# Kernel optimization log

Hardware: AMD Instinct MI355X
Metric: run time of the kernel (lower is better)

## Reference

```python
import jax, jax.numpy as jnp
import numpy as np

NUM_QUBITS = 10
NUM_LAYERS = 5
OBS = 10          # observation_size == num_qubits (required by input_scaling indexing)
NUM_OUTPUTS = 4   # num_actions, discretize=False
BATCH = 4096


def _bcast(theta, n):
    # theta: scalar or (B,) -> broadcastable against (B, 2, 2, ..., 2)
    return jnp.reshape(jnp.asarray(theta), (-1,) + (1,) * n)


def _ry(st, theta, q, n):
    # st: (B,) + (2,)*n complex64; per-sample RY(theta) on qubit q
    t = _bcast(theta, n) * 0.5
    c, s = jnp.cos(t), jnp.sin(t)
    s0 = jax.lax.index_in_dim(st, 0, axis=q + 1, keepdims=True)
    s1 = jax.lax.index_in_dim(st, 1, axis=q + 1, keepdims=True)
    return jnp.concatenate([c * s0 - s * s1, s * s0 + c * s1], axis=q + 1)


def _rz(st, theta, q, n):
    t = _bcast(theta, n) * 0.5
    s0 = jax.lax.index_in_dim(st, 0, axis=q + 1, keepdims=True)
    s1 = jax.lax.index_in_dim(st, 1, axis=q + 1, keepdims=True)
    return jnp.concatenate([jnp.exp(-1j * t) * s0, jnp.exp(1j * t) * s1], axis=q + 1)


def _cnot(st, c, t):
    # flip target axis on the control=1 slab; pure index ops (no residuals in bwd)
    s0 = jax.lax.index_in_dim(st, 0, axis=c + 1, keepdims=True)
    s1 = jax.lax.index_in_dim(st, 1, axis=c + 1, keepdims=True)
    s1 = jnp.flip(s1, axis=t + 1)
    return jnp.concatenate([s0, s1], axis=c + 1)


def _layer(st, x, isc, w, n, obs):
    # isc: (2n,) input_scaling row, w: (2n,) weights row
    for i in range(obs):
        st = _ry(st, isc[i] * x[:, i], i, n)
        st = _rz(st, isc[i + obs] * x[:, i], i, n)
    for i in range(n):
        st = _rz(st, w[i], i, n)
    for i in range(n):
        st = _ry(st, w[i + n], i, n)
    if n == 2:
        st = _cnot(st, 0, 1)
    else:
        for i in range(n):
            st = _cnot(st, i, (i + 1) % n)
    return st


_layer_ckpt = jax.checkpoint(_layer, static_argnums=(4, 5))


def _circuit(x, input_scaling, weights, n, num_layers, obs, num_outputs):
    B = x.shape[0]
    st = jnp.zeros((B,) + (2,) * n, dtype=jnp.complex64)
    st = st.at[(slice(None),) + (0,) * n].set(1.0)  # |0...0>
    for layer in range(num_layers):
        st = _layer_ckpt(st, x, input_scaling[layer], weights[layer], n, obs)
    probs = jnp.real(st * jnp.conj(st))
    outs = []
    for i in range(num_outputs):
        axes = tuple(a for a in range(1, n + 1) if a != i + 1)
        pi = jnp.sum(probs, axis=axes)  # (B, 2)
        outs.append(pi[:, 0] - pi[:, 1])  # <Z_i>
    return jnp.stack(outs, axis=1)


def setup_inputs() -> dict:
    key = jax.random.key(0)
    k1, k2 = jax.random.split(key)
    x = jax.random.normal(k1, (BATCH, OBS), dtype=jnp.float32)
    input_scaling = jnp.ones((NUM_LAYERS, 2 * NUM_QUBITS), dtype=jnp.float32)
    weights = jax.random.uniform(k2, (NUM_LAYERS, 2 * NUM_QUBITS), minval=-np.pi, maxval=np.pi, dtype=jnp.float32)
    output_scaling = jnp.ones((NUM_OUTPUTS,), dtype=jnp.float32)
    return {"x": x, "input_scaling": input_scaling, "weights": weights, "output_scaling": output_scaling}


def reference(x, input_scaling, weights, output_scaling):
    z = _circuit(x, input_scaling, weights, NUM_QUBITS, NUM_LAYERS, OBS, NUM_OUTPUTS)
    return z * output_scaling  # (B, num_actions); discretize=False -> actions = scaled expvals
```

## Files before the change

kernel.cpp:

```cpp
#include <hip/hip_runtime.h>


constexpr int NQ  = 10;
constexpr int NL  = 5;
constexpr int OBS = 10;

typedef float f2 __attribute__((ext_vector_type(2)));

__device__ __forceinline__ float readlane_f(float v, int l) {
    return __int_as_float(__builtin_amdgcn_readlane(__float_as_int(v), l));
}
__device__ __forceinline__ float bperm_f(int byte_addr, float v) {
    return __int_as_float(__builtin_amdgcn_ds_bpermute(byte_addr, __float_as_int(v)));
}
template <int CTRL>
__device__ __forceinline__ float dpp_f(float v) {
    return __int_as_float(__builtin_amdgcn_update_dpp(
        0, __float_as_int(v), CTRL, 0xF, 0xF, true));
}
__device__ __forceinline__ float xor_lane(float v, int M,
                                          int a4, int a16, int a32) {
    switch (M) {
    case 1:  return dpp_f<0xB1>(v);
    case 2:  return dpp_f<0x4E>(v);
    case 8:  return dpp_f<0x128>(v);
    case 4:  return bperm_f(a4,  v);
    case 16: return bperm_f(a16, v);
    default: return bperm_f(a32, v);
    }
}

__global__ __launch_bounds__(256, 4) void qsim_kernel(
    const float* __restrict__ x,
    const float* __restrict__ isc,
    const float* __restrict__ w,
    const float* __restrict__ oscale,
    float* __restrict__ out,
    int B)
{
    const int lane = threadIdx.x & 63;
    const int wid  = (blockIdx.x * blockDim.x + threadIdx.x) >> 6;
    if (wid >= B) return;

    float cUR, cUI, cVR, cVI;
    {
        const int g   = (lane < 50) ? lane : 49;
        const int q   = g % 10;
        const int lyr = g / 10;
        const float xq    = x[wid * OBS + q];
        const float alpha = isc[lyr * 2 * NQ + q]      * xq;
        const float beta  = isc[lyr * 2 * NQ + NQ + q] * xq;
        const float gamma = w[lyr * 2 * NQ + q];
        const float delta = w[lyr * 2 * NQ + NQ + q];
        float sa, ca, sp, cp, sd, cd;
        __sincosf(0.5f * alpha,          &sa, &ca);
        __sincosf(0.5f * (beta + gamma), &sp, &cp);
        __sincosf(0.5f * delta,          &sd, &cd);
        const float A = cd * ca, Bt = sd * sa;
        const float C = cd * sa, D  = sd * ca;
        cUR = (A - Bt) * cp;
        cUI = -(A + Bt) * sp;
        cVR = (C + D) * cp;
        cVI = (C - D) * sp;
    }

    const int a4  = (lane ^ 4)  * 4;
    const int a16 = (lane ^ 16) * 4;
    const int a32 = (lane ^ 32) * 4;
    const int cnot_src  = (lane ^ (lane >> 1));
    const int addr_even = cnot_src * 4;
    const int addr_odd  = (cnot_src ^ 32) * 4;

    f2 c[16];
#pragma unroll
    for (int r = 0; r < 16; ++r) c[r] = (f2){0.f, 0.f};
    c[0].x = (lane == 0) ? 1.f : 0.f;

#define SWAPR(i, j) { f2 _t = c[i]; c[i] = c[j]; c[j] = _t; }

    for (int layer = 0; layer < NL; ++layer) {
        const int base = layer * NQ;

#pragma unroll
        for (int q = 0; q < NQ; ++q) {
            const float ur = readlane_f(cUR, base + q);
            const float ui = readlane_f(cUI, base + q);
            const float vr = readlane_f(cVR, base + q);
            const float vi = readlane_f(cVI, base + q);

            if (q < 4) {
                const f2 kUU  = {ur, ur};
                const f2 kUIm = {-ui, ui};
                const f2 kVVn = {-vr, -vr};
                const f2 kVV  = {vr, vr};
                const f2 kVIm = {-vi, vi};
                const f2 kUIp = {ui, -ui};
                const int m = 1 << (3 - q);
#pragma unroll
                for (int r0 = 0; r0 < 16; ++r0) {
                    if (r0 & m) continue;
                    const int r1 = r0 | m;
                    const f2 c0 = c[r0], c1 = c[r1];
                    const f2 c0s = c0.yx, c1s = c1.yx;
                    c[r0] = kUU*c0 + kUIm*c0s + kVVn*c1 + kVIm*c1s;
                    c[r1] = kVV*c0 + kVIm*c0s + kUU*c1  + kUIp*c1s;
                }
            } else {
                const int  M   = 1 << (9 - q);
                const bool bit = (lane & M) != 0;
                const float Pi = bit ? -ui : ui;
                const float Qr = bit ?  vr : -vr;
                const f2 kUU = {ur, ur};
                const f2 kPI = {-Pi, Pi};
                const f2 kQR = {Qr, Qr};
                const f2 kVI = {-vi, vi};
#pragma unroll
                for (int r = 0; r < 16; ++r) {
                    const f2 mv = c[r];
                    f2 pv;
                    pv.x = xor_lane(mv.x, M, a4, a16, a32);
                    pv.y = xor_lane(mv.y, M, a4, a16, a32);
                    c[r] = kUU*mv + kPI*mv.yx + kQR*pv + kVI*pv.yx;
                }
            }
        }

        SWAPR(8, 12) SWAPR(9, 13) SWAPR(10, 14) SWAPR(11, 15)
        SWAPR(4, 6)  SWAPR(5, 7)  SWAPR(12, 14) SWAPR(13, 15)
        SWAPR(2, 3)  SWAPR(6, 7)  SWAPR(10, 11) SWAPR(14, 15)
#pragma unroll
        for (int r = 0; r < 16; ++r) {
            const int addr = (r & 1) ? addr_odd : addr_even;
            c[r].x = bperm_f(addr, c[r].x);
            c[r].y = bperm_f(addr, c[r].y);
        }
        {
            const bool ctl = (lane & 1) != 0;
#pragma unroll
            for (int r = 0; r < 8; ++r) {
                const f2 t0 = c[r], t1 = c[r + 8];
                c[r]     = ctl ? t1 : t0;
                c[r + 8] = ctl ? t0 : t1;
            }
        }
    }

    float z0 = 0.f, z1 = 0.f, z2 = 0.f, z3 = 0.f;
#pragma unroll
    for (int r = 0; r < 16; ++r) {
        const float pv = c[r].x * c[r].x + c[r].y * c[r].y;
        z0 += (r & 8) ? -pv : pv;
        z1 += (r & 4) ? -pv : pv;
        z2 += (r & 2) ? -pv : pv;
        z3 += (r & 1) ? -pv : pv;
    }
#pragma unroll
    for (int m = 1; m < 64; m <<= 1) {
        z0 += xor_lane(z0, m, a4, a16, a32);
        z1 += xor_lane(z1, m, a4, a16, a32);
        z2 += xor_lane(z2, m, a4, a16, a32);
        z3 += xor_lane(z3, m, a4, a16, a32);
    }
    if (lane == 0) {
        out[wid * 4 + 0] = z0 * oscale[0];
        out[wid * 4 + 1] = z1 * oscale[1];
        out[wid * 4 + 2] = z2 * oscale[2];
        out[wid * 4 + 3] = z3 * oscale[3];
    }
#undef SWAPR
}

extern "C" void kernel_launch(void* const* d_in, const int* in_sizes, int n_in,
                              void* d_out, int out_size, void* d_ws, size_t ws_size,
                              hipStream_t stream) {
    const float* x      = (const float*)d_in[0];
    const float* isc    = (const float*)d_in[1];
    const float* w      = (const float*)d_in[2];
    const float* oscale = (const float*)d_in[3];
    float* out = (float*)d_out;

    const int B = in_sizes[0] / OBS;
    const int threads = 256;
    const int blocks = (B * 64 + threads - 1) / threads;
    qsim_kernel<<<blocks, threads, 0, stream>>>(x, isc, w, oscale, out, B);
}
```

Baseline: 97.32 us.

## Split each sample's state vector across two wavefronts with LDS exchange

Each sample is now handled by a 128-thread block of two wavefronts. Each wavefront holds half the amplitudes (8 registers instead of 16), and the top qubit's gate is applied through a shared-memory exchange between the two halves. The CNOT control swap on qubit 0 is folded into that exchange, and the final expectation values are combined through shared memory. This halves register pressure and doubles the thread count per sample to raise occupancy and parallelism, at the cost of __syncthreads barriers, LDS traffic and some redundant coefficient computation.

```diff
diff --git a/kernel.cpp b/kernel.cpp
--- a/kernel.cpp
+++ b/kernel.cpp
@@ -30,17 +30,19 @@
     }
 }
 
-__global__ __launch_bounds__(256, 4) void qsim_kernel(
+__global__ __launch_bounds__(128, 8) void qsim_kernel(
     const float* __restrict__ x,
     const float* __restrict__ isc,
     const float* __restrict__ w,
     const float* __restrict__ oscale,
-    float* __restrict__ out,
-    int B)
+    float* __restrict__ out)
 {
+    __shared__ f2    sh[1024];
+    __shared__ float red[8];
+
     const int lane = threadIdx.x & 63;
-    const int wid  = (blockIdx.x * blockDim.x + threadIdx.x) >> 6;
-    if (wid >= B) return;
+    const int h    = threadIdx.x >> 6;
+    const int wid  = blockIdx.x;
 
     float cUR, cUI, cVR, cVI;
     {
@@ -71,33 +73,73 @@
     const int addr_even = cnot_src * 4;
     const int addr_odd  = (cnot_src ^ 32) * 4;
 
-    f2 c[16];
-#pragma unroll
-    for (int r = 0; r < 16; ++r) c[r] = (f2){0.f, 0.f};
-    c[0].x = (lane == 0) ? 1.f : 0.f;
+    f2 c[8];
+#pragma unroll
+    for (int r = 0; r < 8; ++r) c[r] = (f2){0.f, 0.f};
+    if (h == 0) c[0].x = (lane == 0) ? 1.f : 0.f;
 
 #define SWAPR(i, j) { f2 _t = c[i]; c[i] = c[j]; c[j] = _t; }
 
     for (int layer = 0; layer < NL; ++layer) {
         const int base = layer * NQ;
 
-#pragma unroll
-        for (int q = 0; q < NQ; ++q) {
+        {
+            const float ur = readlane_f(cUR, base + 0);
+            const float ui = readlane_f(cUI, base + 0);
+            const float vr = readlane_f(cVR, base + 0);
+            const float vi = readlane_f(cVI, base + 0);
+            const f2 kUU  = {ur, ur};
+            const f2 kUIm = {-ui, ui};
+            const f2 kVVn = {-vr, -vr};
+            const f2 kVV  = {vr, vr};
+            const f2 kVIm = {-vi, vi};
+            const f2 kUIp = {ui, -ui};
+
+#pragma unroll
+            for (int r = 0; r < 8; ++r) sh[h * 512 + r * 64 + lane] = c[r];
+            __syncthreads();
+            f2 p[8];
+#pragma unroll
+            for (int r = 0; r < 8; ++r) p[r] = sh[(1 - h) * 512 + r * 64 + lane];
+            __syncthreads();
+
+            const bool swp = (layer != 0) && ((lane & 1) != 0);
+            if (h == 0) {
+#pragma unroll
+                for (int r = 0; r < 8; ++r) {
+                    const f2 a = c[r], b = p[r];
+                    const f2 X0 = swp ? b : a;
+                    const f2 X1 = swp ? a : b;
+                    c[r] = kUU*X0 + kUIm*X0.yx + kVVn*X1 + kVIm*X1.yx;
+                }
+            } else {
+#pragma unroll
+                for (int r = 0; r < 8; ++r) {
+                    const f2 a = c[r], b = p[r];
+                    const f2 X0 = swp ? a : b;
+                    const f2 X1 = swp ? b : a;
+                    c[r] = kVV*X0 + kVIm*X0.yx + kUU*X1 + kUIp*X1.yx;
+                }
+            }
+        }
+
+#pragma unroll
+        for (int q = 1; q < NQ; ++q) {
             const float ur = readlane_f(cUR, base + q);
             const float ui = readlane_f(cUI, base + q);
             const float vr = readlane_f(cVR, base + q);
             const float vi = readlane_f(cVI, base + q);
+            const f2 kUU  = {ur, ur};
+            const f2 kUIm = {-ui, ui};
+            const f2 kVVn = {-vr, -vr};
+            const f2 kVV  = {vr, vr};
+            const f2 kVIm = {-vi, vi};
+            const f2 kUIp = {ui, -ui};
 
             if (q < 4) {
-                const f2 kUU  = {ur, ur};
-                const f2 kUIm = {-ui, ui};
-                const f2 kVVn = {-vr, -vr};
-                const f2 kVV  = {vr, vr};
-                const f2 kVIm = {-vi, vi};
-                const f2 kUIp = {ui, -ui};
                 const int m = 1 << (3 - q);
 #pragma unroll
-                for (int r0 = 0; r0 < 16; ++r0) {
+                for (int r0 = 0; r0 < 8; ++r0) {
                     if (r0 & m) continue;
                     const int r1 = r0 | m;
                     const f2 c0 = c[r0], c1 = c[r1];
@@ -110,46 +152,38 @@
                 const bool bit = (lane & M) != 0;
                 const float Pi = bit ? -ui : ui;
                 const float Qr = bit ?  vr : -vr;
-                const f2 kUU = {ur, ur};
-                const f2 kPI = {-Pi, Pi};
-                const f2 kQR = {Qr, Qr};
-                const f2 kVI = {-vi, vi};
-#pragma unroll
-                for (int r = 0; r < 16; ++r) {
+                const f2 kUUb = {ur, ur};
+                const f2 kPI  = {-Pi, Pi};
+                const f2 kQR  = {Qr, Qr};
+                const f2 kVIb = {-vi, vi};
+#pragma unroll
+                for (int r = 0; r < 8; ++r) {
                     const f2 mv = c[r];
                     f2 pv;
                     pv.x = xor_lane(mv.x, M, a4, a16, a32);
                     pv.y = xor_lane(mv.y, M, a4, a16, a32);
-                    c[r] = kUU*mv + kPI*mv.yx + kQR*pv + kVI*pv.yx;
+                    c[r] = kUUb*mv + kPI*mv.yx + kQR*pv + kVIb*pv.yx;
                 }
             }
         }
 
-        SWAPR(8, 12) SWAPR(9, 13) SWAPR(10, 14) SWAPR(11, 15)
-        SWAPR(4, 6)  SWAPR(5, 7)  SWAPR(12, 14) SWAPR(13, 15)
-        SWAPR(2, 3)  SWAPR(6, 7)  SWAPR(10, 11) SWAPR(14, 15)
-#pragma unroll
-        for (int r = 0; r < 16; ++r) {
+        if (h) { SWAPR(0, 4) SWAPR(1, 5) SWAPR(2, 6) SWAPR(3, 7) }
+        SWAPR(4, 6) SWAPR(5, 7)
+        SWAPR(2, 3) SWAPR(6, 7)
+#pragma unroll
+        for (int r = 0; r < 8; ++r) {
             const int addr = (r & 1) ? addr_odd : addr_even;
             c[r].x = bperm_f(addr, c[r].x);
             c[r].y = bperm_f(addr, c[r].y);
         }
-        {
-            const bool ctl = (lane & 1) != 0;
-#pragma unroll
-            for (int r = 0; r < 8; ++r) {
-                const f2 t0 = c[r], t1 = c[r + 8];
-                c[r]     = ctl ? t1 : t0;
-                c[r + 8] = ctl ? t0 : t1;
-            }
-        }
-    }
-
+    }
+
+    const float s0 = ((h ^ (lane & 1)) ? -1.f : 1.f);
     float z0 = 0.f, z1 = 0.f, z2 = 0.f, z3 = 0.f;
 #pragma unroll
-    for (int r = 0; r < 16; ++r) {
+    for (int r = 0; r < 8; ++r) {
         const float pv = c[r].x * c[r].x + c[r].y * c[r].y;
-        z0 += (r & 8) ? -pv : pv;
+        z0 += s0 * pv;
         z1 += (r & 4) ? -pv : pv;
         z2 += (r & 2) ? -pv : pv;
         z3 += (r & 1) ? -pv : pv;
@@ -162,10 +196,17 @@
         z3 += xor_lane(z3, m, a4, a16, a32);
     }
     if (lane == 0) {
-        out[wid * 4 + 0] = z0 * oscale[0];
-        out[wid * 4 + 1] = z1 * oscale[1];
-        out[wid * 4 + 2] = z2 * oscale[2];
-        out[wid * 4 + 3] = z3 * oscale[3];
+        red[h * 4 + 0] = z0;
+        red[h * 4 + 1] = z1;
+        red[h * 4 + 2] = z2;
+        red[h * 4 + 3] = z3;
+    }
+    __syncthreads();
+    if (h == 0 && lane == 0) {
+        out[wid * 4 + 0] = (red[0] + red[4]) * oscale[0];
+        out[wid * 4 + 1] = (red[1] + red[5]) * oscale[1];
+        out[wid * 4 + 2] = (red[2] + red[6]) * oscale[2];
+        out[wid * 4 + 3] = (red[3] + red[7]) * oscale[3];
     }
 #undef SWAPR
 }
@@ -180,7 +221,5 @@
     float* out = (float*)d_out;
 
     const int B = in_sizes[0] / OBS;
-    const int threads = 256;
-    const int blocks = (B * 64 + threads - 1) / threads;
-    qsim_kernel<<<blocks, threads, 0, stream>>>(x, isc, w, oscale, out, B);
-}
+    qsim_kernel<<<B, 128, 0, stream>>>(x, isc, w, oscale, out);
+}
```

Result: no change. 99.02 us (+1.7%).

## Build first layer as product state and fold final CNOT ring into readout parities

Applied to the files above, without the earlier changes.

The first layer's single-qubit rotations act on |0…0>, so the state is built directly as a tensor product: each lane computes its phase from qubits 4-9, then qubits 0-3 expand across registers. This removes the butterfly and cross-lane shuffles of layer 0. The last layer's CNOT ring is dropped, and its effect on the Z expectations is absorbed by computing parity-based signs over register and lane bits. In exchange, the readout sign logic becomes more intricate and correctness depends on the parity mapping being exact.

```diff
diff --git a/kernel.cpp b/kernel.cpp
--- a/kernel.cpp
+++ b/kernel.cpp
@@ -72,69 +72,99 @@
     const int addr_odd  = (cnot_src ^ 32) * 4;
 
     f2 c[16];
-#pragma unroll
-    for (int r = 0; r < 16; ++r) c[r] = (f2){0.f, 0.f};
-    c[0].x = (lane == 0) ? 1.f : 0.f;
+
+    {
+        float Lr = 1.f, Li = 0.f;
+#pragma unroll
+        for (int q = 4; q < 10; ++q) {
+            const float ur = readlane_f(cUR, q), ui = readlane_f(cUI, q);
+            const float vr = readlane_f(cVR, q), vi = readlane_f(cVI, q);
+            const int M = 1 << (9 - q);
+            const float fr = (lane & M) ? vr : ur;
+            const float fi = (lane & M) ? vi : ui;
+            const float nr = Lr * fr - Li * fi;
+            const float ni = Lr * fi + Li * fr;
+            Lr = nr; Li = ni;
+        }
+        c[0] = (f2){Lr, Li};
+#pragma unroll
+        for (int r = 1; r < 16; ++r) c[r] = (f2){0.f, 0.f};
+#pragma unroll
+        for (int q = 3; q >= 0; --q) {
+            const int m = 1 << (3 - q);
+            const float ur = readlane_f(cUR, q), ui = readlane_f(cUI, q);
+            const float vr = readlane_f(cVR, q), vi = readlane_f(cVI, q);
+#pragma unroll
+            for (int r0 = 0; r0 < 16; ++r0) {
+                if (r0 >= m) continue;
+                const f2 s = c[r0];
+                c[r0 | m] = (f2){ s.x*vr - s.y*vi, s.x*vi + s.y*vr };
+                c[r0]     = (f2){ s.x*ur - s.y*ui, s.x*ui + s.y*ur };
+            }
+        }
+    }
 
 #define SWAPR(i, j) { f2 _t = c[i]; c[i] = c[j]; c[j] = _t; }
 
     for (int layer = 0; layer < NL; ++layer) {
         const int base = layer * NQ;
 
-#pragma unroll
-        for (int q = 0; q < NQ; ++q) {
-            const float ur = readlane_f(cUR, base + q);
-            const float ui = readlane_f(cUI, base + q);
-            const float vr = readlane_f(cVR, base + q);
-            const float vi = readlane_f(cVI, base + q);
-
-            if (q < 4) {
+        if (layer > 0) {
+#pragma unroll
+            for (int q = 0; q < NQ; ++q) {
+                const float ur = readlane_f(cUR, base + q);
+                const float ui = readlane_f(cUI, base + q);
+                const float vr = readlane_f(cVR, base + q);
+                const float vi = readlane_f(cVI, base + q);
                 const f2 kUU  = {ur, ur};
                 const f2 kUIm = {-ui, ui};
                 const f2 kVVn = {-vr, -vr};
                 const f2 kVV  = {vr, vr};
                 const f2 kVIm = {-vi, vi};
                 const f2 kUIp = {ui, -ui};
-                const int m = 1 << (3 - q);
-#pragma unroll
-                for (int r0 = 0; r0 < 16; ++r0) {
-                    if (r0 & m) continue;
-                    const int r1 = r0 | m;
-                    const f2 c0 = c[r0], c1 = c[r1];
-                    const f2 c0s = c0.yx, c1s = c1.yx;
-                    c[r0] = kUU*c0 + kUIm*c0s + kVVn*c1 + kVIm*c1s;
-                    c[r1] = kVV*c0 + kVIm*c0s + kUU*c1  + kUIp*c1s;
+
+                if (q < 4) {
+                    const int m = 1 << (3 - q);
+#pragma unroll
+                    for (int r0 = 0; r0 < 16; ++r0) {
+                        if (r0 & m) continue;
+                        const int r1 = r0 | m;
+                        const f2 c0 = c[r0], c1 = c[r1];
+                        const f2 c0s = c0.yx, c1s = c1.yx;
+                        c[r0] = kUU*c0 + kUIm*c0s + kVVn*c1 + kVIm*c1s;
+                        c[r1] = kVV*c0 + kVIm*c0s + kUU*c1  + kUIp*c1s;
+                    }
+                } else {
+                    const int  M   = 1 << (9 - q);
+                    const bool bit = (lane & M) != 0;
+                    const float Pi = bit ? -ui : ui;
+                    const float Qr = bit ?  vr : -vr;
+                    const f2 kUUb = {ur, ur};
+                    const f2 kPI  = {-Pi, Pi};
+                    const f2 kQR  = {Qr, Qr};
+                    const f2 kVIb = {-vi, vi};
+#pragma unroll
+                    for (int r = 0; r < 16; ++r) {
+                        const f2 mv = c[r];
+                        f2 pv;
+                        pv.x = xor_lane(mv.x, M, a4, a16, a32);
+                        pv.y = xor_lane(mv.y, M, a4, a16, a32);
+                        c[r] = kUUb*mv + kPI*mv.yx + kQR*pv + kVIb*pv.yx;
+                    }
                 }
-            } else {
-                const int  M   = 1 << (9 - q);
-                const bool bit = (lane & M) != 0;
-                const float Pi = bit ? -ui : ui;
-                const float Qr = bit ?  vr : -vr;
-                const f2 kUU = {ur, ur};
-                const f2 kPI = {-Pi, Pi};
-                const f2 kQR = {Qr, Qr};
-                const f2 kVI = {-vi, vi};
-#pragma unroll
-                for (int r = 0; r < 16; ++r) {
-                    const f2 mv = c[r];
-                    f2 pv;
-                    pv.x = xor_lane(mv.x, M, a4, a16, a32);
-                    pv.y = xor_lane(mv.y, M, a4, a16, a32);
-                    c[r] = kUU*mv + kPI*mv.yx + kQR*pv + kVI*pv.yx;
-                }
-            }
-        }
-
-        SWAPR(8, 12) SWAPR(9, 13) SWAPR(10, 14) SWAPR(11, 15)
-        SWAPR(4, 6)  SWAPR(5, 7)  SWAPR(12, 14) SWAPR(13, 15)
-        SWAPR(2, 3)  SWAPR(6, 7)  SWAPR(10, 11) SWAPR(14, 15)
-#pragma unroll
-        for (int r = 0; r < 16; ++r) {
-            const int addr = (r & 1) ? addr_odd : addr_even;
-            c[r].x = bperm_f(addr, c[r].x);
-            c[r].y = bperm_f(addr, c[r].y);
-        }
-        {
+            }
+        }
+
+        if (layer < NL - 1) {
+            SWAPR(8, 12) SWAPR(9, 13) SWAPR(10, 14) SWAPR(11, 15)
+            SWAPR(4, 6)  SWAPR(5, 7)  SWAPR(12, 14) SWAPR(13, 15)
+            SWAPR(2, 3)  SWAPR(6, 7)  SWAPR(10, 11) SWAPR(14, 15)
+#pragma unroll
+            for (int r = 0; r < 16; ++r) {
+                const int addr = (r & 1) ? addr_odd : addr_even;
+                c[r].x = bperm_f(addr, c[r].x);
+                c[r].y = bperm_f(addr, c[r].y);
+            }
             const bool ctl = (lane & 1) != 0;
 #pragma unroll
             for (int r = 0; r < 8; ++r) {
@@ -145,14 +175,16 @@
         }
     }
 
+    const float sL = (__popc(lane) & 1) ? -1.f : 1.f;
     float z0 = 0.f, z1 = 0.f, z2 = 0.f, z3 = 0.f;
 #pragma unroll
     for (int r = 0; r < 16; ++r) {
-        const float pv = c[r].x * c[r].x + c[r].y * c[r].y;
-        z0 += (r & 8) ? -pv : pv;
-        z1 += (r & 4) ? -pv : pv;
-        z2 += (r & 2) ? -pv : pv;
-        z3 += (r & 1) ? -pv : pv;
+        const float pv  = c[r].x * c[r].x + c[r].y * c[r].y;
+        const float pvl = sL * pv;
+        z0 += (__popc(r & 7)  & 1) ? -pvl : pvl;
+        z1 += (__popc(r & 12) & 1) ? -pv  : pv;
+        z2 += (__popc(r & 14) & 1) ? -pv  : pv;
+        z3 += (__popc(r & 15) & 1) ? -pv  : pv;
     }
 #pragma unroll
     for (int m = 1; m < 64; m <<= 1) {
```

Result: faster. 92.52 us (-4.9%).
